# Kernel tuning notes

Hardware: AMD Instinct MI355X
Metric: run time of the kernel (lower is better)

Reference implementation:

```python
import jax, jax.numpy as jnp
import numpy as np

B, N_H, N = 32, 16, 64
R, REP, NUM_CLS = 1024, 1024, 117
NUM_ITER = 2
T_LIS, K_LIS, W_LIS = 8.3, 12.0, 10.0

# static pair indices: x in [0,n_h), y in [0,n), x != y  -> M = N_H*N - N_H
_xx, _yy = np.meshgrid(np.arange(N_H), np.arange(N), indexing='ij')
_mask = _xx != _yy
X_IDX = jnp.asarray(_xx[_mask], dtype=jnp.int32)  # [M]
Y_IDX = jnp.asarray(_yy[_mask], dtype=jnp.int32)  # [M]
M = int(_mask.sum())


def lis(x):
    # low-grade suppression
    return T_LIS / (1.0 + jnp.exp(K_LIS - W_LIS * x))


def setup_inputs() -> dict:
    key = jax.random.key(0)
    ks = jax.random.split(key, 18)
    s = 0.02
    p = lambda k, shp: (jax.random.normal(k, shp) * s).astype(jnp.float32)
    box_features = jax.random.normal(ks[0], (B, N, R), dtype=jnp.float32)
    box_coords = jax.random.uniform(ks[1], (B, N, 4), dtype=jnp.float32)
    box_labels = jax.random.randint(ks[2], (B, N), 0, NUM_CLS).astype(jnp.int32)
    box_labels = box_labels.at[:, :N_H].set(0)  # first N_H are humans (human_idx=0)
    box_scores = jax.random.uniform(ks[3], (B, N), dtype=jnp.float32)
    return {
        'box_features': box_features, 'box_coords': box_coords,
        'box_labels': box_labels, 'box_scores': box_scores,
        'W1': p(ks[4], (2 * R, REP)), 'b1': jnp.zeros((REP,), jnp.float32),
        'W2': p(ks[5], (REP, REP // 2)), 'b2': jnp.zeros((REP // 2,), jnp.float32),
        'W3': p(ks[6], (REP // 2, 1)), 'b3': jnp.zeros((1,), jnp.float32),
        'Ws': p(ks[7], (R, REP)), 'bs': jnp.zeros((REP,), jnp.float32),
        'Wo': p(ks[8], (R, REP)), 'bo': jnp.zeros((REP,), jnp.float32),
        'Wsu': p(ks[9], (R + REP, R)),
        'Wou': p(ks[10], (R + REP, R)),
    }


def reference(box_features, box_coords, box_labels, box_scores,
              W1, b1, W2, b2, W3, b3, Ws, bs, Wo, bo, Wsu, Wou):
    def per_image(enc, coords, labels, scores):
        # enc: [N, R]
        A = jnp.zeros((N_H, N), enc.dtype)
        for _ in range(NUM_ITER):
            pe = jnp.concatenate([enc[X_IDX], enc[Y_IDX]], axis=1)  # [M, 2R]
            h = jax.nn.relu(pe @ W1 + b1)
            h = jax.nn.relu(h @ W2 + b2)
            w = (h @ W3 + b3)[:, 0]  # [M]
            A = jnp.zeros((N_H, N), enc.dtype).at[X_IDX, Y_IDX].set(jax.nn.sigmoid(w))
            msg_h = A @ jax.nn.relu(enc @ Wo + bo)                      # [N_H, REP]
            enc_h = jnp.concatenate([enc[:N_H], msg_h], axis=1) @ Wsu  # [N_H, R]
            enc = enc.at[:N_H].set(enc_h)
            msg_o = A.T @ jax.nn.relu(enc_h @ Ws + bs)                  # [N, REP]
            enc = jnp.concatenate([enc, msg_o], axis=1) @ Wou           # [N, R]
        pair = jnp.concatenate([enc[X_IDX], enc[Y_IDX]], axis=1)  # [M, 2R]
        prod = lis(scores[X_IDX]) * lis(scores[Y_IDX])            # [M]
        # identity object_class_to_target_class: class c -> [c]
        prior = jnp.zeros((M, NUM_CLS), enc.dtype).at[jnp.arange(M), labels[Y_IDX]].set(prod)
        prior = A[X_IDX, Y_IDX][:, None] * prior
        return pair, coords[X_IDX], coords[Y_IDX], prior

    pair, bh, bo_, prior = jax.vmap(per_image)(box_features, box_coords, box_labels, box_scores)
    return (pair.reshape(B * M, 2 * R), bh, bo_, prior.reshape(B * M, NUM_CLS))
```

## Files before the change

### kernel.cpp

```cpp
#include <hip/hip_runtime.h>

#define B_   32
#define N_   64
#define NH   16
#define R_   1024
#define REP  1024
#define M_   1008
#define BM   (B_ * M_)
#define NCLS 117

#define MD_DIRECT 0
#define MD_CC1    2

typedef short bhalf8 __attribute__((ext_vector_type(8)));
typedef float f32x4  __attribute__((ext_vector_type(4)));

typedef __attribute__((address_space(3))) void       lds_t;
typedef const __attribute__((address_space(1))) void gbl_t;
__device__ __forceinline__ void gld16(const void* g, void* l)
{
    __builtin_amdgcn_global_load_lds((gbl_t*)g, (lds_t*)l, 16, 0, 0);
}

__device__ __forceinline__ int xcd_swz(int orig, int q)
{
    return (orig & 7) * q + (orig >> 3);
}
__device__ __forceinline__ int xcd_swz_gen(int orig, int q, int r)
{
    int x = orig & 7, o = orig >> 3;
    return (x < r ? x * (q + 1) : r * (q + 1) + (x - r) * q) + o;
}

__device__ __forceinline__ unsigned short f2bf(float f)
{
    union { float f; unsigned int u; } x; x.f = f;
    unsigned int r = x.u + 0x7FFFu + ((x.u >> 16) & 1u);
    return (unsigned short)(r >> 16);
}
__device__ __forceinline__ float bf2f(unsigned short u)
{
    union { unsigned int i; float f; } x; x.i = ((unsigned int)u) << 16; return x.f;
}

__device__ __forceinline__ unsigned int addrelu2(unsigned int a, unsigned int b)
{
    union { unsigned int u; float f; } la, ha, lb, hb;
    la.u = a << 16;          ha.u = a & 0xffff0000u;
    lb.u = b << 16;          hb.u = b & 0xffff0000u;
    float lo = fmaxf(la.f + lb.f, 0.f);
    float hi = fmaxf(ha.f + hb.f, 0.f);
    unsigned int r;
    asm("v_cvt_pk_bf16_f32 %0, %1, %2" : "=v"(r) : "v"(lo), "v"(hi));
    return r;
}

__device__ __forceinline__ void wait_vm(int n)
{
    if (n >= 8)      asm volatile("s_waitcnt vmcnt(8)" ::: "memory");
    else if (n == 6) asm volatile("s_waitcnt vmcnt(6)" ::: "memory");
    else if (n == 4) asm volatile("s_waitcnt vmcnt(4)" ::: "memory");
    else if (n == 3) asm volatile("s_waitcnt vmcnt(3)" ::: "memory");
    else if (n == 2) asm volatile("s_waitcnt vmcnt(2)" ::: "memory");
    else             asm volatile("s_waitcnt vmcnt(0)" ::: "memory");
}
__device__ __forceinline__ void wait_vm_lgkm(int n)
{
    if (n >= 12)     asm volatile("s_waitcnt vmcnt(12) lgkmcnt(0)" ::: "memory");
    else if (n >= 8) asm volatile("s_waitcnt vmcnt(8) lgkmcnt(0)" ::: "memory");
    else if (n >= 4) asm volatile("s_waitcnt vmcnt(4) lgkmcnt(0)" ::: "memory");
    else             asm volatile("s_waitcnt vmcnt(0) lgkmcnt(0)" ::: "memory");
}

__device__ __forceinline__ void tr32(const float* in, unsigned short* out,
                                     int K, int N, int local)
{
    __shared__ float t[32][33];
    int kb = K >> 5;
    int k0 = (local % kb) * 32, n0 = (local / kb) * 32;
    int tx = threadIdx.x & 31, ty = threadIdx.x >> 5;
#pragma unroll
    for (int r = 0; r < 4; ++r)
        t[ty + r * 8][tx] = in[(size_t)(k0 + ty + r * 8) * N + n0 + tx];
    __syncthreads();
    unsigned int* o32 = (unsigned int*)(out + (size_t)n0 * K + k0);
#pragma unroll
    for (int w = 0; w < 2; ++w) {
        int u = threadIdx.x * 2 + w;
        int n = u >> 4, c = (u & 15) * 2;
        unsigned int val = (unsigned)f2bf(t[c][n]) | ((unsigned)f2bf(t[c + 1][n]) << 16);
        o32[(size_t)n * (K >> 1) + (u & 15)] = val;
    }
}

__global__ __launch_bounds__(256)
void prep_all(const float* __restrict__ W1, const float* __restrict__ W2,
              const float* __restrict__ Wo, const float* __restrict__ Ws,
              const float* __restrict__ Wsu, const float* __restrict__ Wou,
              const float* __restrict__ bo_, const float* __restrict__ b1_,
              const float* __restrict__ feat,
              unsigned short* __restrict__ Wfused, unsigned short* __restrict__ W2t,
              unsigned short* __restrict__ Wst, unsigned short* __restrict__ Wsut,
              unsigned short* __restrict__ Wout, float* __restrict__ biasFull,
              unsigned short* __restrict__ enc0bf)
{
    int bx = blockIdx.x;
    if      (bx < 1024) tr32(W1 + 1024 * 1024, Wfused,               1024, 1024, bx);
    else if (bx < 2048) tr32(Wo,               Wfused + 1024 * 1024, 1024, 1024, bx - 1024);
    else if (bx < 3072) tr32(W1,               Wfused + 2048 * 1024, 1024, 1024, bx - 2048);
    else if (bx < 3584) tr32(W2,  W2t,  1024, 512,  bx - 3072);
    else if (bx < 4608) tr32(Ws,  Wst,  1024, 1024, bx - 3584);
    else if (bx < 6656) tr32(Wsu, Wsut, 2048, 1024, bx - 4608);
    else if (bx < 8704) tr32(Wou, Wout, 2048, 1024, bx - 6656);
    else if (bx < 8716) {
        int c = (bx - 8704) * 256 + threadIdx.x;
        float v = 0.f;
        if (c >= 2048)      v = b1_[c - 2048];
        else if (c >= 1024) v = bo_[c - 1024];
        biasFull[c] = v;
    } else {
        int i = (bx - 8716) * 256 + threadIdx.x;
        float4 a = ((const float4*)feat)[2 * i];
        float4 b = ((const float4*)feat)[2 * i + 1];
        uint4 o;
        o.x = (unsigned)f2bf(a.x) | ((unsigned)f2bf(a.y) << 16);
        o.y = (unsigned)f2bf(a.z) | ((unsigned)f2bf(a.w) << 16);
        o.z = (unsigned)f2bf(b.x) | ((unsigned)f2bf(b.y) << 16);
        o.w = (unsigned)f2bf(b.z) | ((unsigned)f2bf(b.w) << 16);
        ((uint4*)enc0bf)[i] = o;
    }
}

__global__ __launch_bounds__(256)
void gemm_uvgo(const unsigned short* __restrict__ enc,
               const unsigned short* __restrict__ Wf,
               const float* __restrict__ biasFull, unsigned short* __restrict__ XX)
{
    __shared__ unsigned short As[3][128 * 32];
    __shared__ unsigned short Bs[3][128 * 32];
    const int tid  = threadIdx.x;
    const int lane = tid & 63, wave = tid >> 6;
    const int wm = wave & 1, wn = wave >> 1;
    const int l15 = lane & 15, lk = lane >> 4;
    const int wgid = xcd_swz(blockIdx.x, 36);
    const int uSec = wgid >= 256;
    int row0, col0;
    if (!uSec) { row0 = (wgid & 15) * 128;       col0 = (wgid >> 4) * 128; }
    else       { int idx = wgid - 256;
                 row0 = (idx & 3) * 128;         col0 = 2048 + (idx >> 2) * 128; }
    const int kq = (lane & 3) * 8;

    const unsigned short* pA[2];
    const unsigned short* pB[2];
    int ldsOff[2];
#pragma unroll
    for (int i = 0; i < 2; ++i) {
        int tr = wave * 32 + (lane >> 2) + i * 16;
        int grow;
        if (!uSec) grow = row0 + tr;
        else { int hr = row0 + tr; grow = (hr >> 4) * 64 + (hr & 15); }
        pA[i]  = enc + (size_t)grow * 1024 + kq;
        pB[i]  = Wf  + (size_t)(col0 + tr) * 1024 + kq;
        ldsOff[i] = wave * 1024 + i * 512 + lane * 8;
    }

#define STG_UV(slot, k0) do {                          \
        gld16(pA[0] + (k0), &As[slot][ldsOff[0]]);     \
        gld16(pA[1] + (k0), &As[slot][ldsOff[1]]);     \
        gld16(pB[0] + (k0), &Bs[slot][ldsOff[0]]);     \
        gld16(pB[1] + (k0), &Bs[slot][ldsOff[1]]); } while (0)

    f32x4 acc[4][4];
#pragma unroll
    for (int i = 0; i < 4; ++i)
#pragma unroll
    for (int j = 0; j < 4; ++j) acc[i][j] = (f32x4)0.f;

    STG_UV(0, 0);
    STG_UV(1, 32);
    for (int t = 0; t < 32; ++t) {
        const int slot = t % 3;
        if (t + 2 < 32) STG_UV((t + 2) % 3, (t + 2) * 32);
        wait_vm(t < 30 ? 8 : (t == 30 ? 4 : 0));
        __builtin_amdgcn_s_barrier();
        __builtin_amdgcn_sched_barrier(0);
        bhalf8 af[4], bf4[4];
#pragma unroll
        for (int mt = 0; mt < 4; ++mt)
            af[mt] = *(bhalf8*)&As[slot][(wm * 64 + mt * 16 + l15) * 32 + lk * 8];
#pragma unroll
        for (int nt = 0; nt < 4; ++nt)
            bf4[nt] = *(bhalf8*)&Bs[slot][(wn * 64 + nt * 16 + l15) * 32 + lk * 8];
#pragma unroll
        for (int mt = 0; mt < 4; ++mt)
#pragma unroll
        for (int nt = 0; nt < 4; ++nt)
            acc[mt][nt] = __builtin_amdgcn_mfma_f32_16x16x32_bf16(af[mt], bf4[nt],
                                                                  acc[mt][nt], 0, 0, 0);
        __builtin_amdgcn_sched_barrier(0);
        __builtin_amdgcn_s_barrier();
    }
#undef STG_UV

#pragma unroll
    for (int mt = 0; mt < 4; ++mt)
#pragma unroll
    for (int r = 0; r < 4; ++r) {
        int lrow = row0 + wm * 64 + mt * 16 + lk * 4 + r;
        int row = uSec ? ((lrow >> 4) * 64 + (lrow & 15)) : lrow;
#pragma unroll
        for (int nt = 0; nt < 4; ++nt) {
            int col = col0 + wn * 64 + nt * 16 + l15;
            float v = acc[mt][nt][r] + biasFull[col];
            if ((col >> 10) == 1) v = fmaxf(v, 0.f);
            XX[(size_t)row * 3072 + col] = f2bf(v);
        }
    }
}

__global__ __launch_bounds__(512)
void pair_bf(const unsigned short* __restrict__ XX,
             const unsigned short* __restrict__ W2t, const float* __restrict__ b2,
             const float* __restrict__ W3f, float* __restrict__ wpart)
{
    __shared__ unsigned short As[128 * 32];
    __shared__ unsigned short Bs[3][512 * 32];
    __shared__ float red[4][128];
    const int tid  = threadIdx.x;
    const int lane = tid & 63, wave = tid >> 6;
    const int wm = wave & 1, wn = wave >> 1;
    const int l15 = lane & 15, lk = lane >> 4;
    const int wgid = xcd_swz_gen(blockIdx.x, 31, 4);
    const int row0 = wgid * 128;

    const int srow = tid >> 2, skq = (tid & 3) * 8;
    int rg = row0 + srow;
    int b  = rg / M_, m = rg % M_;
    int x  = m / 63, jj = m % 63;
    int y  = jj + (jj >= x ? 1 : 0);
    const unsigned short* Up = XX + ((size_t)(b * 64 + x)) * 3072 + 2048 + skq;
    const unsigned short* Vp = XX + ((size_t)(b * 64 + y)) * 3072 + skq;
    unsigned short* AsW = As + srow * 32 + skq;

    const int kq = (lane & 3) * 8;
    const unsigned short* pB[4];
    int bO[4];
#pragma unroll
    for (int i = 0; i < 4; ++i) {
        int trB = wave * 64 + i * 16 + (lane >> 2);
        pB[i] = W2t + (size_t)trB * REP + kq;
        bO[i] = wave * 2048 + i * 512 + lane * 8;
    }

#define STG_B(slot, k0) do {                        \
        gld16(pB[0] + (k0), &Bs[slot][bO[0]]);      \
        gld16(pB[1] + (k0), &Bs[slot][bO[1]]);      \
        gld16(pB[2] + (k0), &Bs[slot][bO[2]]);      \
        gld16(pB[3] + (k0), &Bs[slot][bO[3]]); } while (0)

    f32x4 acc[4][8];
#pragma unroll
    for (int i = 0; i < 4; ++i)
#pragma unroll
    for (int j = 0; j < 8; ++j) acc[i][j] = (f32x4)0.f;

    uint4 cu = *(const uint4*)(Up);
    uint4 cv = *(const uint4*)(Vp);
    STG_B(0, 0);
    STG_B(1, 32);

    for (int t = 0; t < 32; ++t) {
        const int slot = t % 3;
        const int kn = (t + 1 < 32) ? (t + 1) * 32 : 0;
        uint4 nu = *(const uint4*)(Up + kn);
        uint4 nv = *(const uint4*)(Vp + kn);
        if (t + 2 < 32) STG_B((t + 2) % 3, (t + 2) * 32);

        uint4 h;
        h.x = addrelu2(cu.x, cv.x); h.y = addrelu2(cu.y, cv.y);
        h.z = addrelu2(cu.z, cv.z); h.w = addrelu2(cu.w, cv.w);
        *(uint4*)AsW = h;

        wait_vm_lgkm(t < 30 ? 12 : (t == 30 ? 8 : 4));
        __builtin_amdgcn_s_barrier();
        __builtin_amdgcn_sched_barrier(0);
        bhalf8 af[4], bf4[8];
#pragma unroll
        for (int mt = 0; mt < 4; ++mt)
            af[mt] = *(bhalf8*)&As[(wm * 64 + mt * 16 + l15) * 32 + lk * 8];
#pragma unroll
        for (int nt = 0; nt < 8; ++nt)
            bf4[nt] = *(bhalf8*)&Bs[slot][(wn * 128 + nt * 16 + l15) * 32 + lk * 8];
#pragma unroll
        for (int mt = 0; mt < 4; ++mt)
#pragma unroll
        for (int nt = 0; nt < 8; ++nt)
            acc[mt][nt] = __builtin_amdgcn_mfma_f32_16x16x32_bf16(af[mt], bf4[nt],
                                                                  acc[mt][nt], 0, 0, 0);
        __builtin_amdgcn_sched_barrier(0);
        __builtin_amdgcn_s_barrier();
        cu = nu; cv = nv;
    }
#undef STG_B

    float b2v[8], w3v[8];
#pragma unroll
    for (int nt = 0; nt < 8; ++nt) {
        int col = wn * 128 + nt * 16 + l15;
        b2v[nt] = b2[col];
        w3v[nt] = W3f[col];
    }
#pragma unroll
    for (int mt = 0; mt < 4; ++mt)
#pragma unroll
    for (int r = 0; r < 4; ++r) {
        int rloc = wm * 64 + mt * 16 + lk * 4 + r;
        float p = 0.f;
#pragma unroll
        for (int nt = 0; nt < 8; ++nt)
            p += fmaxf(acc[mt][nt][r] + b2v[nt], 0.f) * w3v[nt];
        p += __shfl_xor(p, 1); p += __shfl_xor(p, 2);
        p += __shfl_xor(p, 4); p += __shfl_xor(p, 8);
        if (l15 == 0) red[wn][rloc] = p;
    }
    __syncthreads();
    if (tid < 128)
        wpart[row0 + tid] = red[0][tid] + red[1][tid] + red[2][tid] + red[3][tid];
}

__device__ __forceinline__ void compute_A(const float* __restrict__ wpart, float b3v,
                                          int b, float* Al, int t)
{
    for (int i = t; i < NH * N_; i += 128) {
        int y = i & 63, x = i >> 6;
        float v = 0.f;
        if (y != x) {
            int j = y - (y > x ? 1 : 0);
            float s = b3v + wpart[b * M_ + x * 63 + j];
            v = 1.f / (1.f + expf(-s));
        }
        Al[i] = v;
    }
}

__global__ __launch_bounds__(128)
void msgh_kernel(const float* __restrict__ wpart, const float* __restrict__ b3,
                 const unsigned short* __restrict__ XX,
                 unsigned short* __restrict__ msgh)
{
    __shared__ float Al[NH * N_];
    __shared__ float Gl[N_][128];
    const int wgid = xcd_swz(blockIdx.x, 32);
    int b = wgid >> 3, c0 = (wgid & 7) * 128, t = threadIdx.x;
    compute_A(wpart, b3[0], b, Al, t);
    for (int y = 0; y < N_; ++y)
        Gl[y][t] = bf2f(XX[((size_t)(b * 64 + y)) * 3072 + 1024 + c0 + t]);
    __syncthreads();
    for (int x = 0; x < NH; ++x) {
        float s = 0.f;
#pragma unroll 8
        for (int y = 0; y < N_; ++y) s += Al[x * N_ + y] * Gl[y][t];
        msgh[((size_t)(b * NH + x)) * REP + c0 + t] = f2bf(s);
    }
}

__global__ __launch_bounds__(256)
void gemm_small(const unsigned short* __restrict__ A1, const unsigned short* __restrict__ A2,
                const unsigned short* __restrict__ Bt, const float* __restrict__ bias,
                unsigned short* __restrict__ Cb, int K, int Nc, int doRelu, int mode)
{
    __shared__ unsigned short As[4][64 * 32];
    __shared__ unsigned short Bs[4][64 * 32];
    const int tid  = threadIdx.x;
    const int lane = tid & 63, wave = tid >> 6;
    const int wr = wave & 1, wc = wave >> 1;
    const int l15 = lane & 15, lk = lane >> 4;
    const int wgid = xcd_swz(blockIdx.x, 16);
    const int row0 = (wgid & 7) * 64, col0 = (wgid >> 3) * 64;
    const int kq = (lane & 3) * 8;

    int tr = wave * 16 + (lane >> 2);
    int rr = row0 + tr;
    const unsigned short* p1;
    const unsigned short* p2 = nullptr;
    if (mode == MD_DIRECT) {
        p1 = A1 + (size_t)rr * K;
    } else {
        int b = rr >> 4, x = rr & 15;
        p1 = A1 + (size_t)(b * 64 + x) * 1024;
        p2 = A2 + (size_t)rr * 1024 - 1024;
    }
    const unsigned short* pA1 = p1 + kq;
    const unsigned short* pA2 = p2 ? p2 + kq : nullptr;
    const unsigned short* pB  = Bt + (size_t)(col0 + tr) * K + kq;
    const int stO = wave * 512 + lane * 8;
    const int kSw = (mode != MD_DIRECT) ? 1024 : K;
    const int NT = K >> 5;

#define STG_MID(slot, k0) do {                                  \
        const unsigned short* ap = ((k0) < kSw) ? pA1 : pA2;    \
        gld16(ap + (k0), &As[slot][stO]);                       \
        gld16(pB + (k0), &Bs[slot][stO]); } while (0)

    f32x4 acc[2][2];
#pragma unroll
    for (int i = 0; i < 2; ++i)
#pragma unroll
    for (int j = 0; j < 2; ++j) acc[i][j] = (f32x4)0.f;

    STG_MID(0, 0);
    STG_MID(1, 32);
    STG_MID(2, 64);
    for (int t = 0; t < NT; ++t) {
        const int slot = t & 3;
        if (t + 3 < NT) STG_MID((t + 3) & 3, (t + 3) * 32);
        int rem = NT - 1 - t;
        wait_vm(rem >= 3 ? 6 : rem * 2);
        __builtin_amdgcn_s_barrier();
        __builtin_amdgcn_sched_barrier(0);
        bhalf8 af[2], bf4[2];
#pragma unroll
        for (int mt = 0; mt < 2; ++mt)
            af[mt] = *(bhalf8*)&As[slot][(wr * 32 + mt * 16 + l15) * 32 + lk * 8];
#pragma unroll
        for (int nt = 0; nt < 2; ++nt)
            bf4[nt] = *(bhalf8*)&Bs[slot][(wc * 32 + nt * 16 + l15) * 32 + lk * 8];
#pragma unroll
        for (int mt = 0; mt < 2; ++mt)
#pragma unroll
        for (int nt = 0; nt < 2; ++nt)
            acc[mt][nt] = __builtin_amdgcn_mfma_f32_16x16x32_bf16(af[mt], bf4[nt],
                                                                  acc[mt][nt], 0, 0, 0);
        __builtin_amdgcn_sched_barrier(0);
        __builtin_amdgcn_s_barrier();
    }
#undef STG_MID

#pragma unroll
    for (int mt = 0; mt < 2; ++mt)
#pragma unroll
    for (int r = 0; r < 4; ++r) {
        int row = row0 + wr * 32 + mt * 16 + lk * 4 + r;
#pragma unroll
        for (int nt = 0; nt < 2; ++nt) {
            int col = col0 + wc * 32 + nt * 16 + l15;
            float v = acc[mt][nt][r];
            if (bias) v += bias[col];
            if (doRelu) v = fmaxf(v, 0.f);
            Cb[(size_t)row * Nc + col] = f2bf(v);
        }
    }
}

__global__ __launch_bounds__(256)
void gemm_cc2(const unsigned short* __restrict__ enc,
              const unsigned short* __restrict__ ench,
              const unsigned short* __restrict__ Gs,
              const unsigned short* __restrict__ Wout,
              const float* __restrict__ wpart, const float* __restrict__ b3,
              float* __restrict__ Cf, unsigned short* __restrict__ Cb)
{
    __shared__ unsigned short As[3][64 * 32];
    __shared__ unsigned short Bt[3][64 * 32];
    __shared__ unsigned short Bb[3][64 * 32];
    __shared__ unsigned short GsL[16][1056];
    __shared__ float Al[16][64];
    __shared__ float gsl[16][68];

    const int tid  = threadIdx.x;
    const int lane = tid & 63, wave = tid >> 6;
    const int wr = wave & 1, wc = wave >> 1;
    const int l15 = lane & 15, lk = lane >> 4;
    const int wgid = xcd_swz(blockIdx.x, 64);
    const int b = wgid >> 4, col0 = (wgid & 15) * 64;
    const int kq = (lane & 3) * 8;

#pragma unroll
    for (int j = 0; j < 8; ++j) {
        int idx = j * 256 + tid;
        int row = idx >> 7, c8 = (idx & 127) * 8;
        uint4 v = *(const uint4*)(Gs + ((size_t)(b * 16 + row)) * 1024 + c8);
        *(uint4*)&GsL[row][c8] = v;
    }
    float b3v = b3[0];
#pragma unroll
    for (int j = 0; j < 4; ++j) {
        int i = j * 256 + tid;
        int y = i & 63, x = i >> 6;
        float v = 0.f;
        if (y != x) {
            int jj = y - (y > x ? 1 : 0);
            float s = b3v + wpart[b * M_ + x * 63 + jj];
            v = 1.f / (1.f + expf(-s));
        }
        Al[x][y] = v;
    }
    asm volatile("s_waitcnt lgkmcnt(0)" ::: "memory");

    int tr = wave * 16 + (lane >> 2);
    const unsigned short* pA = (tr < 16 ? ench + ((size_t)(b * 16 + tr)) * 1024
                                        : enc  + ((size_t)(b * 64 + tr)) * 1024) + kq;
    const unsigned short* pBt = Wout + (size_t)(col0 + tr) * 2048 + kq;
    const unsigned short* pBb = pBt + 1024;
    const int stO = wave * 512 + lane * 8;

#define STG_C2(slot, k0) do {                      \
        gld16(pA  + (k0), &As[slot][stO]);         \
        gld16(pBt + (k0), &Bt[slot][stO]);         \
        gld16(pBb + (k0), &Bb[slot][stO]); } while (0)

    f32x4 acc[2][2];
    f32x4 accg[2];
#pragma unroll
    for (int i = 0; i < 2; ++i) {
        accg[i] = (f32x4)0.f;
#pragma unroll
        for (int j = 0; j < 2; ++j) acc[i][j] = (f32x4)0.f;
    }

    STG_C2(0, 0);
    STG_C2(1, 32);
    for (int t = 0; t < 32; ++t) {
        const int slot = t % 3;
        if (t + 2 < 32) STG_C2((t + 2) % 3, (t + 2) * 32);
        wait_vm(t < 30 ? 6 : (t == 30 ? 3 : 0));
        __builtin_amdgcn_s_barrier();
        __builtin_amdgcn_sched_barrier(0);
        bhalf8 af[2], bt4[2], bb4[2], ags;
#pragma unroll
        for (int mt = 0; mt < 2; ++mt)
            af[mt] = *(bhalf8*)&As[slot][(wr * 32 + mt * 16 + l15) * 32 + lk * 8];
#pragma unroll
        for (int nt = 0; nt < 2; ++nt) {
            bt4[nt] = *(bhalf8*)&Bt[slot][(wc * 32 + nt * 16 + l15) * 32 + lk * 8];
            bb4[nt] = *(bhalf8*)&Bb[slot][(wc * 32 + nt * 16 + l15) * 32 + lk * 8];
        }
        ags = *(bhalf8*)&GsL[l15][t * 32 + lk * 8];
#pragma unroll
        for (int mt = 0; mt < 2; ++mt)
#pragma unroll
        for (int nt = 0; nt < 2; ++nt)
            acc[mt][nt] = __builtin_amdgcn_mfma_f32_16x16x32_bf16(af[mt], bt4[nt],
                                                                  acc[mt][nt], 0, 0, 0);
#pragma unroll
        for (int nt = 0; nt < 2; ++nt)
            accg[nt] = __builtin_amdgcn_mfma_f32_16x16x32_bf16(ags, bb4[nt],
                                                               accg[nt], 0, 0, 0);
        __builtin_amdgcn_sched_barrier(0);
        __builtin_amdgcn_s_barrier();
    }
#undef STG_C2

    if (wr == 0) {
#pragma unroll
        for (int nt = 0; nt < 2; ++nt)
#pragma unroll
        for (int r = 0; r < 4; ++r)
            gsl[lk * 4 + r][wc * 32 + nt * 16 + l15] = accg[nt][r];
    }
    __syncthreads();

#pragma unroll
    for (int x = 0; x < 16; ++x) {
        float g0 = gsl[x][wc * 32 + l15];
        float g1 = gsl[x][wc * 32 + 16 + l15];
#pragma unroll
        for (int mt = 0; mt < 2; ++mt)
#pragma unroll
        for (int r = 0; r < 4; ++r) {
            float a = Al[x][wr * 32 + mt * 16 + lk * 4 + r];
            acc[mt][0][r] += a * g0;
            acc[mt][1][r] += a * g1;
        }
    }
#pragma unroll
    for (int mt = 0; mt < 2; ++mt)
#pragma unroll
    for (int r = 0; r < 4; ++r) {
        size_t row = (size_t)b * 64 + wr * 32 + mt * 16 + lk * 4 + r;
#pragma unroll
        for (int nt = 0; nt < 2; ++nt) {
            int col = col0 + wc * 32 + nt * 16 + l15;
            float v = acc[mt][nt][r];
            if (Cf) Cf[row * 1024 + col] = v;
            else    Cb[row * 1024 + col] = f2bf(v);
        }
    }
}

__device__ __forceinline__ float lis_f(float x)
{
    return 8.3f / (1.f + expf(12.f - 10.f * x));
}

__global__ __launch_bounds__(256)
void outputs_all(const float* __restrict__ enc, const float* __restrict__ coords,
                 const float* __restrict__ wpart, const float* __restrict__ b3,
                 const int* __restrict__ labels, const float* __restrict__ scores,
                 float* __restrict__ out0, float* __restrict__ out1,
                 float* __restrict__ out2, float* __restrict__ out3)
{
    int bx = blockIdx.x;
    if (bx < 64512) {
        int i = bx * 256 + threadIdx.x;
        int r = i >> 9, q = i & 511;
        int b = r / M_, m = r % M_;
        int x = m / 63, j = m % 63;
        int y = j + (j >= x ? 1 : 0);
        const float4* e4 = (const float4*)enc;
        float4 v = (q < 256) ? e4[(b * 64 + x) * 256 + q]
                             : e4[(b * 64 + y) * 256 + (q - 256)];
        ((float4*)out0)[i] = v;
    } else if (bx < 64638) {
        int r = (bx - 64512) * 256 + threadIdx.x;
        int b = r / M_, m = r % M_;
        int x = m / 63, j = m % 63;
        int y = j + (j >= x ? 1 : 0);
        const float4* c4 = (const float4*)coords;
        ((float4*)out1)[r] = c4[b * 64 + x];
        ((float4*)out2)[r] = c4[b * 64 + y];
    } else {
        int i = (bx - 64638) * 256 + threadIdx.x;
        int r = i / NCLS, c = i % NCLS;
        int b = r / M_, m = r % M_;
        int x = m / 63, j = m % 63;
        int y = j + (j >= x ? 1 : 0);
        int lab = labels[b * 64 + y];
        float val = 0.f;
        if (c == lab) {
            float w = b3[0] + wpart[r];
            float A = 1.f / (1.f + expf(-w));
            float sx = scores[b * 64 + x], sy = scores[b * 64 + y];
            val = A * lis_f(sx) * lis_f(sy);
        }
        out3[i] = val;
    }
}

extern "C" void kernel_launch(void* const* d_in, const int* in_sizes, int n_in,
                              void* d_out, int out_size, void* d_ws, size_t ws_size,
                              hipStream_t stream)
{
    const float* box_features = (const float*)d_in[0];
    const float* box_coords   = (const float*)d_in[1];
    const int*   box_labels   = (const int*)d_in[2];
    const float* box_scores   = (const float*)d_in[3];
    const float* W1  = (const float*)d_in[4];
    const float* b1  = (const float*)d_in[5];
    const float* W2  = (const float*)d_in[6];
    const float* b2  = (const float*)d_in[7];
    const float* W3  = (const float*)d_in[8];
    const float* b3  = (const float*)d_in[9];
    const float* Ws  = (const float*)d_in[10];
    const float* bs  = (const float*)d_in[11];
    const float* Wo  = (const float*)d_in[12];
    const float* bo  = (const float*)d_in[13];
    const float* Wsu = (const float*)d_in[14];
    const float* Wou = (const float*)d_in[15];

    float* wsf  = (float*)d_ws;
    float* encA = wsf;           wsf += (size_t)B_ * N_ * R_;
    float* wpart= wsf;           wsf += (size_t)BM;
    float* biasFull = wsf;       wsf += 3072;

    unsigned short* wsu = (unsigned short*)wsf;
    unsigned short* enc0bf = wsu;  wsu += (size_t)B_ * N_ * R_;
    unsigned short* encIbf = wsu;  wsu += (size_t)B_ * N_ * R_;
    unsigned short* XX     = wsu;  wsu += (size_t)B_ * N_ * 3072;
    unsigned short* msghbf = wsu;  wsu += (size_t)B_ * NH * REP;
    unsigned short* enchbf = wsu;  wsu += (size_t)B_ * NH * R_;
    unsigned short* Gsbf   = wsu;  wsu += (size_t)B_ * NH * REP;
    unsigned short* Wfused = wsu;  wsu += (size_t)3072 * 1024;
    unsigned short* W2t    = wsu;  wsu += (size_t)512 * 1024;
    unsigned short* Wst    = wsu;  wsu += (size_t)1024 * 1024;
    unsigned short* Wsut   = wsu;  wsu += (size_t)1024 * 2048;
    unsigned short* Wout   = wsu;  wsu += (size_t)1024 * 2048;

    float* out0 = (float*)d_out;
    float* out1 = out0 + (size_t)BM * 2048;
    float* out2 = out1 + (size_t)BM * 4;
    float* out3 = out2 + (size_t)BM * 4;

    prep_all<<<9740, 256, 0, stream>>>(W1, W2, Wo, Ws, Wsu, Wou, bo, b1, box_features,
                                       Wfused, W2t, Wst, Wsut, Wout, biasFull, enc0bf);

    for (int it = 0; it < 2; ++it) {
        const unsigned short* enc = (it == 0) ? enc0bf : encIbf;
        gemm_uvgo<<<288, 256, 0, stream>>>(enc, Wfused, biasFull, XX);
        pair_bf<<<252, 512, 0, stream>>>(XX, W2t, b2, W3, wpart);
        msgh_kernel<<<256, 128, 0, stream>>>(wpart, b3, XX, msghbf);
        gemm_small<<<128, 256, 0, stream>>>(enc, msghbf, Wsut, nullptr,
                                            enchbf, 2048, 1024, 0, MD_CC1);
        gemm_small<<<128, 256, 0, stream>>>(enchbf, nullptr, Wst, bs,
                                            Gsbf, 1024, 1024, 1, MD_DIRECT);
        gemm_cc2<<<512, 256, 0, stream>>>(enc, enchbf, Gsbf, Wout, wpart, b3,
                                          (it == 1) ? encA : nullptr,
                                          (it == 0) ? encIbf : nullptr);
    }

    outputs_all<<<79380, 256, 0, stream>>>(encA, box_coords, wpart, b3,
                                           box_labels, box_scores,
                                           out0, out1, out2, out3);
}
```

Before: 662.9 us.

## Interleave LDS reads, prefetch and MFMA phases in pair_bf with double-buffered A

Restructures the pair_bf main loop into four phases. Each phase loads two B fragments, issues one global-to-LDS prefetch and runs a block of MFMAs under s_setprio, with barriers between phases. The A tile is double-buffered so the next step's add+relu result can be written while the current one is still being read. The aim is to hide LDS and global latency behind MFMA work, at the cost of more barriers per iteration and twice the LDS used for A.

```diff
diff --git a/kernel.cpp b/kernel.cpp
--- a/kernel.cpp
+++ b/kernel.cpp
@@ -63,13 +63,6 @@
     else if (n == 3) asm volatile("s_waitcnt vmcnt(3)" ::: "memory");
     else if (n == 2) asm volatile("s_waitcnt vmcnt(2)" ::: "memory");
     else             asm volatile("s_waitcnt vmcnt(0)" ::: "memory");
-}
-__device__ __forceinline__ void wait_vm_lgkm(int n)
-{
-    if (n >= 12)     asm volatile("s_waitcnt vmcnt(12) lgkmcnt(0)" ::: "memory");
-    else if (n >= 8) asm volatile("s_waitcnt vmcnt(8) lgkmcnt(0)" ::: "memory");
-    else if (n >= 4) asm volatile("s_waitcnt vmcnt(4) lgkmcnt(0)" ::: "memory");
-    else             asm volatile("s_waitcnt vmcnt(0) lgkmcnt(0)" ::: "memory");
 }
 
 __device__ __forceinline__ void tr32(const float* in, unsigned short* out,
@@ -223,7 +216,7 @@
              const unsigned short* __restrict__ W2t, const float* __restrict__ b2,
              const float* __restrict__ W3f, float* __restrict__ wpart)
 {
-    __shared__ unsigned short As[128 * 32];
+    __shared__ unsigned short As[2][128 * 32];
     __shared__ unsigned short Bs[3][512 * 32];
     __shared__ float red[4][128];
     const int tid  = threadIdx.x;
@@ -240,7 +233,7 @@
     int y  = jj + (jj >= x ? 1 : 0);
     const unsigned short* Up = XX + ((size_t)(b * 64 + x)) * 3072 + 2048 + skq;
     const unsigned short* Vp = XX + ((size_t)(b * 64 + y)) * 3072 + skq;
-    unsigned short* AsW = As + srow * 32 + skq;
+    const int aw = srow * 32 + skq;
 
     const int kq = (lane & 3) * 8;
     const unsigned short* pB[4];
@@ -252,56 +245,102 @@
         bO[i] = wave * 2048 + i * 512 + lane * 8;
     }
 
-#define STG_B(slot, k0) do {                        \
-        gld16(pB[0] + (k0), &Bs[slot][bO[0]]);      \
-        gld16(pB[1] + (k0), &Bs[slot][bO[1]]);      \
-        gld16(pB[2] + (k0), &Bs[slot][bO[2]]);      \
-        gld16(pB[3] + (k0), &Bs[slot][bO[3]]); } while (0)
-
     f32x4 acc[4][8];
 #pragma unroll
     for (int i = 0; i < 4; ++i)
 #pragma unroll
     for (int j = 0; j < 8; ++j) acc[i][j] = (f32x4)0.f;
+
+#define MFMA_PAIR(n0, n1)                                                       \
+    do {                                                                        \
+        _Pragma("unroll")                                                       \
+        for (int mt = 0; mt < 4; ++mt) {                                        \
+            acc[mt][n0] = __builtin_amdgcn_mfma_f32_16x16x32_bf16(af[mt], bq0,  \
+                                                         acc[mt][n0], 0, 0, 0); \
+            acc[mt][n1] = __builtin_amdgcn_mfma_f32_16x16x32_bf16(af[mt], bq1,  \
+                                                         acc[mt][n1], 0, 0, 0); \
+        }                                                                       \
+    } while (0)
+
+#define PHASE_MFMA(n0, n1)                              \
+    do {                                                \
+        __builtin_amdgcn_s_barrier();                   \
+        asm volatile("s_waitcnt lgkmcnt(0)" ::: "memory"); \
+        __builtin_amdgcn_sched_barrier(0);              \
+        __builtin_amdgcn_s_setprio(1);                  \
+        MFMA_PAIR(n0, n1);                              \
+        __builtin_amdgcn_s_setprio(0);                  \
+        __builtin_amdgcn_sched_barrier(0);              \
+        __builtin_amdgcn_s_barrier();                   \
+    } while (0)
 
     uint4 cu = *(const uint4*)(Up);
     uint4 cv = *(const uint4*)(Vp);
-    STG_B(0, 0);
-    STG_B(1, 32);
-
-    for (int t = 0; t < 32; ++t) {
-        const int slot = t % 3;
-        const int kn = (t + 1 < 32) ? (t + 1) * 32 : 0;
-        uint4 nu = *(const uint4*)(Up + kn);
-        uint4 nv = *(const uint4*)(Vp + kn);
-        if (t + 2 < 32) STG_B((t + 2) % 3, (t + 2) * 32);
-
+#pragma unroll
+    for (int i = 0; i < 4; ++i) gld16(pB[i], &Bs[0][bO[i]]);
+#pragma unroll
+    for (int i = 0; i < 4; ++i) gld16(pB[i] + 32, &Bs[1][bO[i]]);
+    asm volatile("s_waitcnt vmcnt(8)" ::: "memory");
+    {
         uint4 h;
         h.x = addrelu2(cu.x, cv.x); h.y = addrelu2(cu.y, cv.y);
         h.z = addrelu2(cu.z, cv.z); h.w = addrelu2(cu.w, cv.w);
-        *(uint4*)AsW = h;
-
-        wait_vm_lgkm(t < 30 ? 12 : (t == 30 ? 8 : 4));
+        *(uint4*)&As[0][aw] = h;
+    }
+    asm volatile("s_waitcnt vmcnt(4) lgkmcnt(0)" ::: "memory");
+    __builtin_amdgcn_s_barrier();
+
+    for (int t = 0; t < 32; ++t) {
+        const unsigned short* Bc = Bs[t % 3];
+        unsigned short* Bn = (unsigned short*)Bs[(t + 2) % 3];
+        const unsigned short* Ac = As[t & 1];
+        const bool pf = (t + 2 < 32);
+        const int k2 = (t + 2) * 32;
+        const int kn = (t + 1 < 32) ? (t + 1) * 32 : 0;
+
+        bhalf8 af[4];
+#pragma unroll
+        for (int mt = 0; mt < 4; ++mt)
+            af[mt] = *(bhalf8*)&Ac[(wm * 64 + mt * 16 + l15) * 32 + lk * 8];
+
+        bhalf8 bq0 = *(bhalf8*)&Bc[(wn * 128 + 0 * 16 + l15) * 32 + lk * 8];
+        bhalf8 bq1 = *(bhalf8*)&Bc[(wn * 128 + 1 * 16 + l15) * 32 + lk * 8];
+        if (pf) gld16(pB[0] + k2, &Bn[bO[0]]);
+        uint4 nu = *(const uint4*)(Up + kn);
+        uint4 nv = *(const uint4*)(Vp + kn);
+        PHASE_MFMA(0, 1);
+
+        bq0 = *(bhalf8*)&Bc[(wn * 128 + 2 * 16 + l15) * 32 + lk * 8];
+        bq1 = *(bhalf8*)&Bc[(wn * 128 + 3 * 16 + l15) * 32 + lk * 8];
+        if (pf) gld16(pB[1] + k2, &Bn[bO[1]]);
+        PHASE_MFMA(2, 3);
+
+        bq0 = *(bhalf8*)&Bc[(wn * 128 + 4 * 16 + l15) * 32 + lk * 8];
+        bq1 = *(bhalf8*)&Bc[(wn * 128 + 5 * 16 + l15) * 32 + lk * 8];
+        if (pf) gld16(pB[2] + k2, &Bn[bO[2]]);
+        PHASE_MFMA(4, 5);
+
+        bq0 = *(bhalf8*)&Bc[(wn * 128 + 6 * 16 + l15) * 32 + lk * 8];
+        bq1 = *(bhalf8*)&Bc[(wn * 128 + 7 * 16 + l15) * 32 + lk * 8];
+        if (pf) gld16(pB[3] + k2, &Bn[bO[3]]);
+        {
+            uint4 h;
+            h.x = addrelu2(nu.x, nv.x); h.y = addrelu2(nu.y, nv.y);
+            h.z = addrelu2(nu.z, nv.z); h.w = addrelu2(nu.w, nv.w);
+            *(uint4*)&As[(t + 1) & 1][aw] = h;
+        }
+        if (t < 30) asm volatile("s_waitcnt vmcnt(3) lgkmcnt(0)" ::: "memory");
+        else        asm volatile("s_waitcnt vmcnt(0) lgkmcnt(0)" ::: "memory");
         __builtin_amdgcn_s_barrier();
         __builtin_amdgcn_sched_barrier(0);
-        bhalf8 af[4], bf4[8];
-#pragma unroll
-        for (int mt = 0; mt < 4; ++mt)
-            af[mt] = *(bhalf8*)&As[(wm * 64 + mt * 16 + l15) * 32 + lk * 8];
-#pragma unroll
-        for (int nt = 0; nt < 8; ++nt)
-            bf4[nt] = *(bhalf8*)&Bs[slot][(wn * 128 + nt * 16 + l15) * 32 + lk * 8];
-#pragma unroll
-        for (int mt = 0; mt < 4; ++mt)
-#pragma unroll
-        for (int nt = 0; nt < 8; ++nt)
-            acc[mt][nt] = __builtin_amdgcn_mfma_f32_16x16x32_bf16(af[mt], bf4[nt],
-                                                                  acc[mt][nt], 0, 0, 0);
+        __builtin_amdgcn_s_setprio(1);
+        MFMA_PAIR(6, 7);
+        __builtin_amdgcn_s_setprio(0);
         __builtin_amdgcn_sched_barrier(0);
         __builtin_amdgcn_s_barrier();
-        cu = nu; cv = nv;
-    }
-#undef STG_B
+    }
+#undef PHASE_MFMA
+#undef MFMA_PAIR
 
     float b2v[8], w3v[8];
 #pragma unroll
```

Result: no change. 658.7 us (median of 2 runs) (-0.6%).

## Split pair_bf into smaller 64x256 tiles with column halves and partial sums

Applied to the files above, without the earlier changes.

The pair MLP second-layer kernel goes from 128-row by full-512-column tiles on 252 blocks to 64-row by 256-column tiles on 1008 blocks. Each column half writes its own partial W3 dot product into a doubled wpart buffer, and the consumers (compute_A, msgh, outputs) add the two halves. This is meant to fill more of the GPU's compute units and allow several blocks per CU through smaller LDS and register footprints. In exchange, the A-operand (U+V add/relu) loads are repeated for both column halves, and each MFMA step does less work per barrier.

```diff
diff --git a/kernel.cpp b/kernel.cpp
--- a/kernel.cpp
+++ b/kernel.cpp
@@ -26,11 +26,6 @@
 {
     return (orig & 7) * q + (orig >> 3);
 }
-__device__ __forceinline__ int xcd_swz_gen(int orig, int q, int r)
-{
-    int x = orig & 7, o = orig >> 3;
-    return (x < r ? x * (q + 1) : r * (q + 1) + (x - r) * q) + o;
-}
 
 __device__ __forceinline__ unsigned short f2bf(float f)
 {
@@ -63,13 +58,6 @@
     else if (n == 3) asm volatile("s_waitcnt vmcnt(3)" ::: "memory");
     else if (n == 2) asm volatile("s_waitcnt vmcnt(2)" ::: "memory");
     else             asm volatile("s_waitcnt vmcnt(0)" ::: "memory");
-}
-__device__ __forceinline__ void wait_vm_lgkm(int n)
-{
-    if (n >= 12)     asm volatile("s_waitcnt vmcnt(12) lgkmcnt(0)" ::: "memory");
-    else if (n >= 8) asm volatile("s_waitcnt vmcnt(8) lgkmcnt(0)" ::: "memory");
-    else if (n >= 4) asm volatile("s_waitcnt vmcnt(4) lgkmcnt(0)" ::: "memory");
-    else             asm volatile("s_waitcnt vmcnt(0) lgkmcnt(0)" ::: "memory");
 }
 
 __device__ __forceinline__ void tr32(const float* in, unsigned short* out,
@@ -218,83 +206,83 @@
     }
 }
 
-__global__ __launch_bounds__(512)
+__global__ __launch_bounds__(512, 4)
 void pair_bf(const unsigned short* __restrict__ XX,
              const unsigned short* __restrict__ W2t, const float* __restrict__ b2,
              const float* __restrict__ W3f, float* __restrict__ wpart)
 {
-    __shared__ unsigned short As[128 * 32];
-    __shared__ unsigned short Bs[3][512 * 32];
-    __shared__ float red[4][128];
+    __shared__ unsigned short As[64 * 32];
+    __shared__ unsigned short Bs[3][256 * 32];
+    __shared__ float red[4][64];
     const int tid  = threadIdx.x;
     const int lane = tid & 63, wave = tid >> 6;
-    const int wm = wave & 1, wn = wave >> 1;
+    const int wr = wave & 1, wc = wave >> 1;
     const int l15 = lane & 15, lk = lane >> 4;
-    const int wgid = xcd_swz_gen(blockIdx.x, 31, 4);
-    const int row0 = wgid * 128;
-
-    const int srow = tid >> 2, skq = (tid & 3) * 8;
+    const int wgid = xcd_swz(blockIdx.x, 126);
+    const int cx = wgid & 1, ry = wgid >> 1;
+    const int row0 = ry * 64, col0 = cx * 256;
+
+    const int srow = tid >> 3, skq = (tid & 7) * 4;
     int rg = row0 + srow;
     int b  = rg / M_, m = rg % M_;
     int x  = m / 63, jj = m % 63;
     int y  = jj + (jj >= x ? 1 : 0);
     const unsigned short* Up = XX + ((size_t)(b * 64 + x)) * 3072 + 2048 + skq;
     const unsigned short* Vp = XX + ((size_t)(b * 64 + y)) * 3072 + skq;
-    unsigned short* AsW = As + srow * 32 + skq;
+    const int aw = srow * 32 + skq;
 
     const int kq = (lane & 3) * 8;
-    const unsigned short* pB[4];
-    int bO[4];
-#pragma unroll
-    for (int i = 0; i < 4; ++i) {
-        int trB = wave * 64 + i * 16 + (lane >> 2);
-        pB[i] = W2t + (size_t)trB * REP + kq;
-        bO[i] = wave * 2048 + i * 512 + lane * 8;
+    const unsigned short* pB[2];
+    int bO[2];
+#pragma unroll
+    for (int i = 0; i < 2; ++i) {
+        int trB = i * 128 + (tid >> 2);
+        pB[i] = W2t + (size_t)(col0 + trB) * REP + kq;
+        bO[i] = i * 4096 + wave * 512 + lane * 8;
     }
 
 #define STG_B(slot, k0) do {                        \
         gld16(pB[0] + (k0), &Bs[slot][bO[0]]);      \
-        gld16(pB[1] + (k0), &Bs[slot][bO[1]]);      \
-        gld16(pB[2] + (k0), &Bs[slot][bO[2]]);      \
-        gld16(pB[3] + (k0), &Bs[slot][bO[3]]); } while (0)
-
-    f32x4 acc[4][8];
-#pragma unroll
-    for (int i = 0; i < 4; ++i)
-#pragma unroll
-    for (int j = 0; j < 8; ++j) acc[i][j] = (f32x4)0.f;
-
-    uint4 cu = *(const uint4*)(Up);
-    uint4 cv = *(const uint4*)(Vp);
+        gld16(pB[1] + (k0), &Bs[slot][bO[1]]); } while (0)
+
+    f32x4 acc[2][4];
+#pragma unroll
+    for (int i = 0; i < 2; ++i)
+#pragma unroll
+    for (int j = 0; j < 4; ++j) acc[i][j] = (f32x4)0.f;
+
+    uint2 cu = *(const uint2*)(Up);
+    uint2 cv = *(const uint2*)(Vp);
     STG_B(0, 0);
     STG_B(1, 32);
 
     for (int t = 0; t < 32; ++t) {
         const int slot = t % 3;
         const int kn = (t + 1 < 32) ? (t + 1) * 32 : 0;
-        uint4 nu = *(const uint4*)(Up + kn);
-        uint4 nv = *(const uint4*)(Vp + kn);
+        uint2 nu = *(const uint2*)(Up + kn);
+        uint2 nv = *(const uint2*)(Vp + kn);
         if (t + 2 < 32) STG_B((t + 2) % 3, (t + 2) * 32);
 
-        uint4 h;
-        h.x = addrelu2(cu.x, cv.x); h.y = addrelu2(cu.y, cv.y);
-        h.z = addrelu2(cu.z, cv.z); h.w = addrelu2(cu.w, cv.w);
-        *(uint4*)AsW = h;
-
-        wait_vm_lgkm(t < 30 ? 12 : (t == 30 ? 8 : 4));
-        __builtin_amdgcn_s_barrier();
-        __builtin_amdgcn_sched_barrier(0);
-        bhalf8 af[4], bf4[8];
-#pragma unroll
-        for (int mt = 0; mt < 4; ++mt)
-            af[mt] = *(bhalf8*)&As[(wm * 64 + mt * 16 + l15) * 32 + lk * 8];
-#pragma unroll
-        for (int nt = 0; nt < 8; ++nt)
-            bf4[nt] = *(bhalf8*)&Bs[slot][(wn * 128 + nt * 16 + l15) * 32 + lk * 8];
-#pragma unroll
-        for (int mt = 0; mt < 4; ++mt)
-#pragma unroll
-        for (int nt = 0; nt < 8; ++nt)
+        uint2 h;
+        h.x = addrelu2(cu.x, cv.x);
+        h.y = addrelu2(cu.y, cv.y);
+        *(uint2*)&As[aw] = h;
+
+        if (t < 31) asm volatile("s_waitcnt vmcnt(6) lgkmcnt(0)" ::: "memory");
+        else        asm volatile("s_waitcnt vmcnt(0) lgkmcnt(0)" ::: "memory");
+        __builtin_amdgcn_s_barrier();
+        __builtin_amdgcn_sched_barrier(0);
+        bhalf8 af[2], bf4[4];
+#pragma unroll
+        for (int mt = 0; mt < 2; ++mt)
+            af[mt] = *(bhalf8*)&As[(wr * 32 + mt * 16 + l15) * 32 + lk * 8];
+#pragma unroll
+        for (int nt = 0; nt < 4; ++nt)
+            bf4[nt] = *(bhalf8*)&Bs[slot][(wc * 64 + nt * 16 + l15) * 32 + lk * 8];
+#pragma unroll
+        for (int mt = 0; mt < 2; ++mt)
+#pragma unroll
+        for (int nt = 0; nt < 4; ++nt)
             acc[mt][nt] = __builtin_amdgcn_mfma_f32_16x16x32_bf16(af[mt], bf4[nt],
                                                                   acc[mt][nt], 0, 0, 0);
         __builtin_amdgcn_sched_barrier(0);
@@ -303,29 +291,30 @@
     }
 #undef STG_B
 
-    float b2v[8], w3v[8];
-#pragma unroll
-    for (int nt = 0; nt < 8; ++nt) {
-        int col = wn * 128 + nt * 16 + l15;
+    float b2v[4], w3v[4];
+#pragma unroll
+    for (int nt = 0; nt < 4; ++nt) {
+        int col = col0 + wc * 64 + nt * 16 + l15;
         b2v[nt] = b2[col];
         w3v[nt] = W3f[col];
     }
 #pragma unroll
-    for (int mt = 0; mt < 4; ++mt)
+    for (int mt = 0; mt < 2; ++mt)
 #pragma unroll
     for (int r = 0; r < 4; ++r) {
-        int rloc = wm * 64 + mt * 16 + lk * 4 + r;
+        int rloc = wr * 32 + mt * 16 + lk * 4 + r;
         float p = 0.f;
 #pragma unroll
-        for (int nt = 0; nt < 8; ++nt)
+        for (int nt = 0; nt < 4; ++nt)
             p += fmaxf(acc[mt][nt][r] + b2v[nt], 0.f) * w3v[nt];
         p += __shfl_xor(p, 1); p += __shfl_xor(p, 2);
         p += __shfl_xor(p, 4); p += __shfl_xor(p, 8);
-        if (l15 == 0) red[wn][rloc] = p;
+        if (l15 == 0) red[wc][rloc] = p;
     }
     __syncthreads();
-    if (tid < 128)
-        wpart[row0 + tid] = red[0][tid] + red[1][tid] + red[2][tid] + red[3][tid];
+    if (tid < 64)
+        wpart[cx * BM + row0 + tid] = red[0][tid] + red[1][tid]
+                                    + red[2][tid] + red[3][tid];
 }
 
 __device__ __forceinline__ void compute_A(const float* __restrict__ wpart, float b3v,
@@ -336,7 +325,8 @@
         float v = 0.f;
         if (y != x) {
             int j = y - (y > x ? 1 : 0);
-            float s = b3v + wpart[b * M_ + x * 63 + j];
+            int r = b * M_ + x * 63 + j;
+            float s = b3v + wpart[r] + wpart[BM + r];
             v = 1.f / (1.f + expf(-s));
         }
         Al[i] = v;
@@ -490,7 +480,8 @@
         float v = 0.f;
         if (y != x) {
             int jj = y - (y > x ? 1 : 0);
-            float s = b3v + wpart[b * M_ + x * 63 + jj];
+            int r = b * M_ + x * 63 + jj;
+            float s = b3v + wpart[r] + wpart[BM + r];
             v = 1.f / (1.f + expf(-s));
         }
         Al[x][y] = v;
@@ -628,7 +619,7 @@
         int lab = labels[b * 64 + y];
         float val = 0.f;
         if (c == lab) {
-            float w = b3[0] + wpart[r];
+            float w = b3[0] + wpart[r] + wpart[BM + r];
             float A = 1.f / (1.f + expf(-w));
             float sx = scores[b * 64 + x], sy = scores[b * 64 + y];
             val = A * lis_f(sx) * lis_f(sy);
@@ -660,7 +651,7 @@
 
     float* wsf  = (float*)d_ws;
     float* encA = wsf;           wsf += (size_t)B_ * N_ * R_;
-    float* wpart= wsf;           wsf += (size_t)BM;
+    float* wpart= wsf;           wsf += (size_t)2 * BM;
     float* biasFull = wsf;       wsf += 3072;
 
     unsigned short* wsu = (unsigned short*)wsf;
@@ -687,7 +678,7 @@
     for (int it = 0; it < 2; ++it) {
         const unsigned short* enc = (it == 0) ? enc0bf : encIbf;
         gemm_uvgo<<<288, 256, 0, stream>>>(enc, Wfused, biasFull, XX);
-        pair_bf<<<252, 512, 0, stream>>>(XX, W2t, b2, W3, wpart);
+        pair_bf<<<1008, 512, 0, stream>>>(XX, W2t, b2, W3, wpart);
         msgh_kernel<<<256, 128, 0, stream>>>(wpart, b3, XX, msghbf);
         gemm_small<<<128, 256, 0, stream>>>(enc, msghbf, Wsut, nullptr,
                                             enchbf, 2048, 1024, 0, MD_CC1);
```

Result: slower. 676.3 us (+2.0%).
